# Optimization experiments

Measured on AMD Instinct MI355X. Metric: run time of the kernel, lower is better.

## Reference

```python
import jax, jax.numpy as jnp
import numpy as np

B, S, HID = 2, 2048, 2048
H, D = 16, 128        # num_heads, kv_channels
LAYER_IDX = 4
MASK_VALUE = -10000.0


def setup_inputs() -> dict:
    key = jax.random.key(0)
    ks = jax.random.split(key, 5)
    hidden_states = jax.random.normal(ks[0], (B, S, HID), dtype=jnp.float32)
    # causal mask, broadcastable to [B, q, H, k] per torch.where(mask, w, mask_value)
    causal = jnp.tril(jnp.ones((S, S), dtype=bool))
    attention_mask = jnp.broadcast_to(causal[None, :, None, :], (B, S, 1, S))
    Wq = jax.random.normal(ks[1], (HID, H * D), dtype=jnp.float32) * (HID ** -0.5)
    bq = jnp.zeros((H * D,), dtype=jnp.float32)
    Wkv = jax.random.normal(ks[2], (HID, 2 * D), dtype=jnp.float32) * (HID ** -0.5)
    bkv = jnp.zeros((2 * D,), dtype=jnp.float32)
    Wp = jax.random.normal(ks[3], (H * D, HID), dtype=jnp.float32) * ((H * D) ** -0.5)
    bp = jnp.zeros((HID,), dtype=jnp.float32)
    return {"hidden_states": hidden_states, "attention_mask": attention_mask,
            "Wq": Wq, "bq": bq, "Wkv": Wkv, "bkv": bkv, "Wp": Wp, "bp": bp}


def reference(hidden_states, attention_mask, Wq, bq, Wkv, bkv, Wp, bp):
    # projections
    q = hidden_states @ Wq + bq                      # [B,S,H*D]
    kv = hidden_states @ Wkv + bkv                   # [B,S,2D]
    k, v = kv[..., :D], kv[..., D:]                  # shared single K/V head [B,S,D]
    qh = q.reshape(B, S, H, D)
    # baddbmm with alpha = 1/(layer_idx * sqrt(D))
    scale_factor = (1.0 / LAYER_IDX) / (D ** 0.5)
    scores = jnp.einsum('bqhd,bkd->bqhk', qh, k) * scale_factor  # [B,q,H,k]
    # upcast softmax with unscale = layer_idx, masked with -1e4
    scores = scores.astype(jnp.float32) * LAYER_IDX
    scores = jnp.where(attention_mask, scores, MASK_VALUE)
    weights = jax.nn.softmax(scores, axis=-1).astype(hidden_states.dtype)
    attn = jnp.einsum('bqhk,bkd->bqhd', weights, v).reshape(B, S, H * D)
    out = attn @ Wp + bp
    return out
```

## Files before the change

kernel.cpp:

```cpp
#include <hip/hip_runtime.h>

#define DEVI __device__ __forceinline__

typedef unsigned int u32;
typedef unsigned short u16;

constexpr int Bc = 2, Sc = 2048, HIDc = 2048, Hc = 16, Dc = 128;
constexpr int Mrows = Bc * Sc;
constexpr float SCALE = 0.08838834764831845f;
constexpr float M0 = 16.0f;

typedef float f32x4 __attribute__((ext_vector_type(4)));
typedef __bf16 bf16x8 __attribute__((ext_vector_type(8)));

DEVI float bf2f(u16 v) { return __builtin_bit_cast(float, (u32)v << 16); }
DEVI u16 f2bf(float x) {
  u32 u = __builtin_bit_cast(u32, x);
  u32 r = (u + 0x7fffu + ((u >> 16) & 1u)) >> 16;
  return (u16)r;
}

DEVI void async16(void* lds, const void* g) {
  __builtin_amdgcn_global_load_lds((const __attribute__((address_space(1))) void*)g,
                                   (__attribute__((address_space(3))) void*)lds,
                                   16, 0, 0);
}

constexpr int PRE_BLOCKS = 6289;
constexpr int TS = 66;

DEVI void do_transpose64(const void* in, u16* out, int R, int C, int c0, int r0, bool bf,
                         u16* tile, int tid) {
  const int cg = (tid & 7) * 8, ry = tid >> 3;
#pragma unroll
  for (int p = 0; p < 2; ++p) {
    int r = ry + p * 32;
    size_t idx = (size_t)(r0 + r) * C + (c0 + cg);
    u16 tmp[8];
    if (bf) {
      *(uint4*)tmp = *(const uint4*)&((const u16*)in)[idx];
    } else {
      const float* f = (const float*)in + idx;
#pragma unroll
      for (int j = 0; j < 8; ++j) tmp[j] = f2bf(f[j]);
    }
    *(uint4*)&tile[r * TS + cg] = *(const uint4*)tmp;
  }
  __syncthreads();
  const int rx = (tid & 7) * 8, cy = tid >> 3;
#pragma unroll
  for (int p = 0; p < 2; ++p) {
    int c = cy + p * 32;
    u16 tmp[8];
#pragma unroll
    for (int j = 0; j < 8; ++j) tmp[j] = tile[(rx + j) * TS + c];
    *(uint4*)&out[(size_t)(c0 + c) * R + r0 + rx] = *(const uint4*)tmp;
  }
}

__global__ __launch_bounds__(256) void pre_kernel(const void* __restrict__ hs,
                                                  const void* __restrict__ Wq,
                                                  const void* __restrict__ bq,
                                                  const void* __restrict__ Wkv,
                                                  const void* __restrict__ bkv,
                                                  const void* __restrict__ Wp,
                                                  const void* __restrict__ bp,
                                                  u16* __restrict__ HSb, u16* __restrict__ WqT,
                                                  u16* __restrict__ WkvT, u16* __restrict__ WpT,
                                                  u16* __restrict__ biasB, int* __restrict__ flag) {
  __shared__ int cnt;
  __shared__ u16 tile[64 * TS];
  const int tid = threadIdx.x, bx = blockIdx.x;
  if (tid == 0) cnt = 0;
  __syncthreads();
  int ok = 0;
  const u32* hw = (const u32*)hs;
  for (int i = tid; i < 512; i += 256) {
    u32 lo = hw[i] & 0xffffu;
    u32 e = (lo >> 7) & 0xffu;
    if (lo == 0u || (e >= 118u && e <= 134u)) ok++;
  }
  atomicAdd(&cnt, ok);
  __syncthreads();
  const bool bf = cnt > 256;
  if (bx == 0 && tid == 0) *flag = bf ? 1 : 0;

  if (bx < 4096) {
    int i = (bx * 256 + tid) * 8;
    if (bf) {
      *(uint4*)&HSb[i] = *(const uint4*)&((const u16*)hs)[i];
    } else {
      const float* f = (const float*)hs;
      u16 tmp[8];
#pragma unroll
      for (int j = 0; j < 8; ++j) tmp[j] = f2bf(f[i + j]);
      *(uint4*)&HSb[i] = *(const uint4*)tmp;
    }
  } else if (bx < 5120) {
    int t = bx - 4096;
    do_transpose64(Wq, WqT, 2048, 2048, (t & 31) * 64, (t >> 5) * 64, bf, tile, tid);
  } else if (bx < 5248) {
    int t = bx - 5120;
    do_transpose64(Wkv, WkvT, 2048, 256, (t & 3) * 64, (t >> 2) * 64, bf, tile, tid);
  } else if (bx < 6272) {
    int t = bx - 5248;
    do_transpose64(Wp, WpT, 2048, 2048, (t & 31) * 64, (t >> 5) * 64, bf, tile, tid);
  } else {
    int i = (bx - 6272) * 256 + tid;
    if (i < 4352) {
      const void* src;
      int j;
      if (i < 2048) { src = bq; j = i; }
      else if (i < 2304) { src = bkv; j = i - 2048; }
      else { src = bp; j = i - 2304; }
      biasB[i] = bf ? ((const u16*)src)[j] : f2bf(((const float*)src)[j]);
    }
  }
}

__global__ __launch_bounds__(512, 4) void gemm_bt(const u16* __restrict__ A,
                                                  const u16* __restrict__ BT,
                                                  const u16* __restrict__ bias,
                                                  void* __restrict__ C,
                                                  int M, int N, int K,
                                                  const int* __restrict__ flag,
                                                  int mode) {
  __shared__ __align__(16) u16 As[2][128 * 32];
  __shared__ __align__(16) u16 Bs[2][128 * 32];
  const int tid = threadIdx.x;
  const int bm = blockIdx.x, bn = blockIdx.y;
  const int wave = tid >> 6, lane = tid & 63;
  const int wm = (wave & 3) * 32, wn = (wave >> 2) * 64;
  const int lr = lane & 15, kq = lane >> 4;
  f32x4 acc[2][4] = {};
  const size_t a_base = (size_t)bm * 128 * K;
  const size_t b_base = (size_t)bn * 128 * K;

#define STAGE(k0, buf)                                                             \
  {                                                                                \
    int r = tid >> 2, c = tid & 3;                                                 \
    int gc = (c ^ (r & 3)) << 3;                                                   \
    async16(&As[buf][tid * 8], A + a_base + (size_t)r * K + (k0) + gc);            \
    async16(&Bs[buf][tid * 8], BT + b_base + (size_t)r * K + (k0) + gc);           \
  }

  STAGE(0, 0);
  const int nsteps = K >> 5;
  for (int s = 0; s < nsteps; ++s) {
    const int cur = s & 1;
    asm volatile("s_waitcnt vmcnt(0)" ::: "memory");
    asm volatile("s_barrier" ::: "memory");
    if (s + 1 < nsteps) STAGE((s + 1) << 5, cur ^ 1);
    bf16x8 af[2], bfr[4];
#pragma unroll
    for (int i = 0; i < 2; ++i) {
      int ra = wm + i * 16 + lr;
      af[i] = *(const bf16x8*)&As[cur][ra * 32 + ((kq ^ (ra & 3)) << 3)];
    }
#pragma unroll
    for (int i = 0; i < 4; ++i) {
      int rb = wn + i * 16 + lr;
      bfr[i] = *(const bf16x8*)&Bs[cur][rb * 32 + ((kq ^ (rb & 3)) << 3)];
    }
#pragma unroll
    for (int mi = 0; mi < 2; ++mi)
#pragma unroll
      for (int ni = 0; ni < 4; ++ni)
        acc[mi][ni] = __builtin_amdgcn_mfma_f32_16x16x32_bf16(af[mi], bfr[ni], acc[mi][ni], 0, 0, 0);
  }
#undef STAGE

  if (mode == 3) {
    u16* Qout = (u16*)C;
    u16* KsG = Qout + (size_t)4096 * 2048;
    u16* VtG = KsG + (size_t)4096 * 128;
    const bool isQ = (bn < 16);
#pragma unroll
    for (int mi = 0; mi < 2; ++mi)
#pragma unroll
      for (int ni = 0; ni < 4; ++ni) {
        int col = bn * 128 + wn + ni * 16 + lr;
        float bv = bf2f(bias[col]);
#pragma unroll
        for (int rr = 0; rr < 4; ++rr) {
          int row = bm * 128 + wm + mi * 16 + kq * 4 + rr;
          u16 v = f2bf(acc[mi][ni][rr] + bv);
          if (isQ) {
            Qout[(size_t)row * 2048 + col] = v;
          } else {
            int c2 = col - 2048;
            if (c2 < 128) {
              int d = c2;
              KsG[(size_t)row * 128 + (((d >> 3) ^ (row & 15)) << 3) + (d & 7)] = v;
            } else {
              int d = c2 - 128, bb = row >> 11, s = row & 2047;
              VtG[((size_t)(bb * 128 + d)) * 2048 + (s & ~63) +
                  ((((s >> 3) & 7) ^ (d & 7)) << 3) + (s & 7)] = v;
            }
          }
        }
      }
    return;
  }
  const bool out16 = (mode == 0) || (*flag != 0);
#pragma unroll
  for (int mi = 0; mi < 2; ++mi)
#pragma unroll
    for (int ni = 0; ni < 4; ++ni) {
      int col = bn * 128 + wn + ni * 16 + lr;
      float bv = bf2f(bias[col]);
#pragma unroll
      for (int rr = 0; rr < 4; ++rr) {
        int row = bm * 128 + wm + mi * 16 + kq * 4 + rr;
        float v = acc[mi][ni][rr] + bv;
        size_t idx = (size_t)row * N + col;
        if (out16) ((u16*)C)[idx] = f2bf(v);
        else ((float*)C)[idx] = v;
      }
    }
}

constexpr int PS_STRIDE = 72;

__global__ __launch_bounds__(256) void flash_mfma(const u16* __restrict__ Q,
                                                  const u16* __restrict__ KsG,
                                                  const u16* __restrict__ VtG,
                                                  u16* __restrict__ O) {
  __shared__ __align__(16) u16 Ks[2][64 * 128];
  __shared__ __align__(16) u16 Vt[2][128 * 64];
  __shared__ __align__(16) u16 Ps[64 * PS_STRIDE];
  const int pairidx = blockIdx.x, h = blockIdx.y, b = blockIdx.z;
  const int tid = threadIdx.x;
  const int wave = tid >> 6, lane = tid & 63;
  const int lr = lane & 15, kq = lane >> 4;

  for (int half = 0; half < 2; ++half) {
    const int qt = (half == 0) ? pairidx : 31 - pairidx;
    bf16x8 qf[4];
    const u16* qbase = Q + ((size_t)(b * 2048 + qt * 64 + wave * 16 + lr)) * 2048 + h * 128;
#pragma unroll
    for (int kk = 0; kk < 4; ++kk)
      qf[kk] = *(const bf16x8*)(qbase + kk * 32 + kq * 8);
    f32x4 of[8] = {};
    float lsum[4] = {0.f, 0.f, 0.f, 0.f};
    const int srow = qt * 64 + wave * 16 + kq * 4;
    const int kmax = qt * 64;

    {
      const u16* g = KsG + ((size_t)(b * 2048)) * 128;
#pragma unroll
      for (int it = 0; it < 4; ++it)
        async16(&Ks[0][it * 2048 + tid * 8], g + it * 2048 + tid * 8);
      const size_t vbase = ((size_t)b * 128) * 2048;
#pragma unroll
      for (int it = 0; it < 4; ++it) {
        int chunk = it * 256 + tid;
        async16(&Vt[0][chunk * 8], VtG + vbase + (size_t)(chunk >> 3) * 2048 + (chunk & 7) * 8);
      }
    }

    for (int k0 = 0; k0 <= kmax; k0 += 64) {
      const int cur = (k0 >> 6) & 1;
      asm volatile("s_waitcnt vmcnt(0)" ::: "memory");
      asm volatile("s_barrier" ::: "memory");
      if (k0 + 64 <= kmax) {
        const int nxt = cur ^ 1;
        const u16* g = KsG + ((size_t)(b * 2048 + k0 + 64)) * 128;
#pragma unroll
        for (int it = 0; it < 4; ++it)
          async16(&Ks[nxt][it * 2048 + tid * 8], g + it * 2048 + tid * 8);
        const size_t vbase = ((size_t)b * 128) * 2048 + k0 + 64;
#pragma unroll
        for (int it = 0; it < 4; ++it) {
          int chunk = it * 256 + tid;
          async16(&Vt[nxt][chunk * 8], VtG + vbase + (size_t)(chunk >> 3) * 2048 + (chunk & 7) * 8);
        }
      }

      const bool diag = (k0 == kmax);
      f32x4 sf[4] = {};
#pragma unroll
      for (int nt = 0; nt < 4; ++nt) {
        int keyl = nt * 16 + lr;
#pragma unroll
        for (int kk = 0; kk < 4; ++kk) {
          const bf16x8 kf = *(const bf16x8*)&Ks[cur][keyl * 128 + ((((kk << 2) + kq) ^ lr) << 3)];
          sf[nt] = __builtin_amdgcn_mfma_f32_16x16x32_bf16(qf[kk], kf, sf[nt], 0, 0, 0);
        }
      }
#pragma unroll
      for (int nt = 0; nt < 4; ++nt) {
        int t = k0 + nt * 16 + lr;
#pragma unroll
        for (int r = 0; r < 4; ++r) {
          float v = fmaf(sf[nt][r], SCALE, -M0);
          if (diag && t > srow + r) v = -1e30f;
          float p = __expf(v);
          lsum[r] += p;
          Ps[(wave * 16 + kq * 4 + r) * PS_STRIDE + nt * 16 + lr] = f2bf(p);
        }
      }
#pragma unroll
      for (int ks = 0; ks < 2; ++ks) {
        const bf16x8 pf = *(const bf16x8*)&Ps[(wave * 16 + lr) * PS_STRIDE + ks * 32 + kq * 8];
#pragma unroll
        for (int dt = 0; dt < 8; ++dt) {
          int d = dt * 16 + lr;
          const bf16x8 vf = *(const bf16x8*)&Vt[cur][d * 64 + ((((ks << 2) + kq) ^ (d & 7)) << 3)];
          of[dt] = __builtin_amdgcn_mfma_f32_16x16x32_bf16(pf, vf, of[dt], 0, 0, 0);
        }
      }
    }
    float linv[4];
#pragma unroll
    for (int r = 0; r < 4; ++r) {
      float l = lsum[r];
      l += __shfl_xor(l, 1);
      l += __shfl_xor(l, 2);
      l += __shfl_xor(l, 4);
      l += __shfl_xor(l, 8);
      linv[r] = 1.f / l;
    }
    u16* obase = O + ((size_t)(b * 2048 + qt * 64 + wave * 16 + kq * 4)) * 2048 + h * 128;
#pragma unroll
    for (int dt = 0; dt < 8; ++dt)
#pragma unroll
      for (int r = 0; r < 4; ++r)
        obase[(size_t)r * 2048 + dt * 16 + lr] = f2bf(of[dt][r] * linv[r]);
    __syncthreads();
  }
}

extern "C" void kernel_launch(void* const* d_in, const int* in_sizes, int n_in,
                              void* d_out, int out_size, void* d_ws, size_t ws_size,
                              hipStream_t stream) {
  (void)in_sizes; (void)n_in; (void)out_size; (void)ws_size;
  const void* hs  = d_in[0];
  const void* Wq  = d_in[2];
  const void* bq  = d_in[3];
  const void* Wkv = d_in[4];
  const void* bkv = d_in[5];
  const void* Wp  = d_in[6];
  const void* bp  = d_in[7];

  char* ws = (char*)d_ws;
  int* flag  = (int*)(ws + 0);
  u16* HSb   = (u16*)(ws + 256);
  u16* WqT   = (u16*)(ws + 16777472);
  u16* WkvT  = (u16*)(ws + 25166080);
  u16* WpT   = (u16*)(ws + 26214656);
  u16* biasB = (u16*)(ws + 34603264);
  u16* Qb    = (u16*)(ws + 34611968);
  u16* KsG   = (u16*)(ws + 51389184);
  u16* VtG   = (u16*)(ws + 52437760);
  u16* ATTNb = (u16*)(ws + 53486336);

  pre_kernel<<<PRE_BLOCKS, 256, 0, stream>>>(hs, Wq, bq, Wkv, bkv, Wp, bp,
                                             HSb, WqT, WkvT, WpT, biasB, flag);
  gemm_bt<<<dim3(32, 18), 512, 0, stream>>>(HSb, WqT, biasB, Qb, 4096, 2304, 2048, flag, 3);
  flash_mfma<<<dim3(16, 16, 2), 256, 0, stream>>>(Qb, KsG, VtG, ATTNb);
  gemm_bt<<<dim3(32, 16), 512, 0, stream>>>(ATTNb, WpT, biasB + 2304, d_out, 4096, 2048, 2048, flag, 1);
}
```

Before: 311.3 us.

## Enlarge flash attention query tile to 128 rows per block

Each wave now processes two 16-row query slices (32 rows), so a block covers 128 query rows and every K/V tile loaded into LDS feeds twice as many MFMAs. The grid is halved to 8x16x2 blocks with causal pairing adjusted, and the diagonal masking now spans the last two key tiles. This cuts K/V LDS traffic and global reloads per query row, at the cost of doubled accumulator registers (launch_bounds min 1) and fewer blocks for occupancy and load balance.

New measurement: 328.2 us. 1.05x slower.

```diff
diff --git a/kernel.cpp b/kernel.cpp
--- a/kernel.cpp
+++ b/kernel.cpp
@@ -222,29 +222,35 @@
 
 constexpr int PS_STRIDE = 72;
 
-__global__ __launch_bounds__(256) void flash_mfma(const u16* __restrict__ Q,
-                                                  const u16* __restrict__ KsG,
-                                                  const u16* __restrict__ VtG,
-                                                  u16* __restrict__ O) {
+__global__ __launch_bounds__(256, 1) void flash_mfma(const u16* __restrict__ Q,
+                                                     const u16* __restrict__ KsG,
+                                                     const u16* __restrict__ VtG,
+                                                     u16* __restrict__ O) {
   __shared__ __align__(16) u16 Ks[2][64 * 128];
   __shared__ __align__(16) u16 Vt[2][128 * 64];
-  __shared__ __align__(16) u16 Ps[64 * PS_STRIDE];
+  __shared__ __align__(16) u16 Ps[128 * PS_STRIDE];
   const int pairidx = blockIdx.x, h = blockIdx.y, b = blockIdx.z;
   const int tid = threadIdx.x;
   const int wave = tid >> 6, lane = tid & 63;
   const int lr = lane & 15, kq = lane >> 4;
+  const int wm = wave * 32;
 
   for (int half = 0; half < 2; ++half) {
-    const int qt = (half == 0) ? pairidx : 31 - pairidx;
-    bf16x8 qf[4];
-    const u16* qbase = Q + ((size_t)(b * 2048 + qt * 64 + wave * 16 + lr)) * 2048 + h * 128;
-#pragma unroll
-    for (int kk = 0; kk < 4; ++kk)
-      qf[kk] = *(const bf16x8*)(qbase + kk * 32 + kq * 8);
-    f32x4 of[8] = {};
-    float lsum[4] = {0.f, 0.f, 0.f, 0.f};
-    const int srow = qt * 64 + wave * 16 + kq * 4;
-    const int kmax = qt * 64;
+    const int qt = (half == 0) ? pairidx : 15 - pairidx;
+    bf16x8 qf[2][4];
+#pragma unroll
+    for (int mi = 0; mi < 2; ++mi) {
+      const u16* qbase =
+          Q + ((size_t)(b * 2048 + qt * 128 + wm + mi * 16 + lr)) * 2048 + h * 128;
+#pragma unroll
+      for (int kk = 0; kk < 4; ++kk)
+        qf[mi][kk] = *(const bf16x8*)(qbase + kk * 32 + kq * 8);
+    }
+    f32x4 of[2][8] = {};
+    float lsum[2][4] = {{0.f, 0.f, 0.f, 0.f}, {0.f, 0.f, 0.f, 0.f}};
+    const int srow = qt * 128 + wm + kq * 4;
+    const int kmax = qt * 128 + 64;
+    const int diag0 = qt * 128;
 
     {
       const u16* g = KsG + ((size_t)(b * 2048)) * 128;
@@ -273,60 +279,70 @@
 #pragma unroll
         for (int it = 0; it < 4; ++it) {
           int chunk = it * 256 + tid;
-          async16(&Vt[nxt][chunk * 8], VtG + vbase + (size_t)(chunk >> 3) * 2048 + (chunk & 7) * 8);
-        }
-      }
-
-      const bool diag = (k0 == kmax);
-      f32x4 sf[4] = {};
+          async16(&Vt[nxt][chunk * 8],
+                  VtG + vbase + (size_t)(chunk >> 3) * 2048 + (chunk & 7) * 8);
+        }
+      }
+
+      const bool diag = (k0 >= diag0);
+      f32x4 sf[2][4] = {};
 #pragma unroll
       for (int nt = 0; nt < 4; ++nt) {
         int keyl = nt * 16 + lr;
 #pragma unroll
         for (int kk = 0; kk < 4; ++kk) {
           const bf16x8 kf = *(const bf16x8*)&Ks[cur][keyl * 128 + ((((kk << 2) + kq) ^ lr) << 3)];
-          sf[nt] = __builtin_amdgcn_mfma_f32_16x16x32_bf16(qf[kk], kf, sf[nt], 0, 0, 0);
-        }
-      }
-#pragma unroll
-      for (int nt = 0; nt < 4; ++nt) {
-        int t = k0 + nt * 16 + lr;
-#pragma unroll
-        for (int r = 0; r < 4; ++r) {
-          float v = fmaf(sf[nt][r], SCALE, -M0);
-          if (diag && t > srow + r) v = -1e30f;
-          float p = __expf(v);
-          lsum[r] += p;
-          Ps[(wave * 16 + kq * 4 + r) * PS_STRIDE + nt * 16 + lr] = f2bf(p);
-        }
-      }
+          sf[0][nt] = __builtin_amdgcn_mfma_f32_16x16x32_bf16(qf[0][kk], kf, sf[0][nt], 0, 0, 0);
+          sf[1][nt] = __builtin_amdgcn_mfma_f32_16x16x32_bf16(qf[1][kk], kf, sf[1][nt], 0, 0, 0);
+        }
+      }
+#pragma unroll
+      for (int mi = 0; mi < 2; ++mi)
+#pragma unroll
+        for (int nt = 0; nt < 4; ++nt) {
+          int t = k0 + nt * 16 + lr;
+#pragma unroll
+          for (int r = 0; r < 4; ++r) {
+            float v = fmaf(sf[mi][nt][r], SCALE, -M0);
+            if (diag && t > srow + mi * 16 + r) v = -1e30f;
+            float p = __expf(v);
+            lsum[mi][r] += p;
+            Ps[(wm + mi * 16 + kq * 4 + r) * PS_STRIDE + nt * 16 + lr] = f2bf(p);
+          }
+        }
 #pragma unroll
       for (int ks = 0; ks < 2; ++ks) {
-        const bf16x8 pf = *(const bf16x8*)&Ps[(wave * 16 + lr) * PS_STRIDE + ks * 32 + kq * 8];
+        const bf16x8 pf0 = *(const bf16x8*)&Ps[(wm + lr) * PS_STRIDE + ks * 32 + kq * 8];
+        const bf16x8 pf1 = *(const bf16x8*)&Ps[(wm + 16 + lr) * PS_STRIDE + ks * 32 + kq * 8];
 #pragma unroll
         for (int dt = 0; dt < 8; ++dt) {
           int d = dt * 16 + lr;
           const bf16x8 vf = *(const bf16x8*)&Vt[cur][d * 64 + ((((ks << 2) + kq) ^ (d & 7)) << 3)];
-          of[dt] = __builtin_amdgcn_mfma_f32_16x16x32_bf16(pf, vf, of[dt], 0, 0, 0);
-        }
-      }
-    }
-    float linv[4];
-#pragma unroll
-    for (int r = 0; r < 4; ++r) {
-      float l = lsum[r];
-      l += __shfl_xor(l, 1);
-      l += __shfl_xor(l, 2);
-      l += __shfl_xor(l, 4);
-      l += __shfl_xor(l, 8);
-      linv[r] = 1.f / l;
-    }
-    u16* obase = O + ((size_t)(b * 2048 + qt * 64 + wave * 16 + kq * 4)) * 2048 + h * 128;
-#pragma unroll
-    for (int dt = 0; dt < 8; ++dt)
-#pragma unroll
-      for (int r = 0; r < 4; ++r)
-        obase[(size_t)r * 2048 + dt * 16 + lr] = f2bf(of[dt][r] * linv[r]);
+          of[0][dt] = __builtin_amdgcn_mfma_f32_16x16x32_bf16(pf0, vf, of[0][dt], 0, 0, 0);
+          of[1][dt] = __builtin_amdgcn_mfma_f32_16x16x32_bf16(pf1, vf, of[1][dt], 0, 0, 0);
+        }
+      }
+    }
+#pragma unroll
+    for (int mi = 0; mi < 2; ++mi) {
+      float linv[4];
+#pragma unroll
+      for (int r = 0; r < 4; ++r) {
+        float l = lsum[mi][r];
+        l += __shfl_xor(l, 1);
+        l += __shfl_xor(l, 2);
+        l += __shfl_xor(l, 4);
+        l += __shfl_xor(l, 8);
+        linv[r] = 1.f / l;
+      }
+      u16* obase =
+          O + ((size_t)(b * 2048 + qt * 128 + wm + mi * 16 + kq * 4)) * 2048 + h * 128;
+#pragma unroll
+      for (int dt = 0; dt < 8; ++dt)
+#pragma unroll
+        for (int r = 0; r < 4; ++r)
+          obase[(size_t)r * 2048 + dt * 16 + lr] = f2bf(of[mi][dt][r] * linv[r]);
+    }
     __syncthreads();
   }
 }
@@ -358,6 +374,6 @@
   pre_kernel<<<PRE_BLOCKS, 256, 0, stream>>>(hs, Wq, bq, Wkv, bkv, Wp, bp,
                                              HSb, WqT, WkvT, WpT, biasB, flag);
   gemm_bt<<<dim3(32, 18), 512, 0, stream>>>(HSb, WqT, biasB, Qb, 4096, 2304, 2048, flag, 3);
-  flash_mfma<<<dim3(16, 16, 2), 256, 0, stream>>>(Qb, KsG, VtG, ATTNb);
+  flash_mfma<<<dim3(8, 16, 2), 256, 0, stream>>>(Qb, KsG, VtG, ATTNb);
   gemm_bt<<<dim3(32, 16), 512, 0, stream>>>(ATTNb, WpT, biasB + 2304, d_out, 4096, 2048, 2048, flag, 1);
 }
```

## Keep softmax probabilities in registers via transposed QK MFMA and permuted V layout

Applied to the files above, without the earlier changes.

Swaps the MFMA operand order for QK^T so each lane holds scores for one query row across keys, which lets the probabilities be packed into bf16 registers and fed directly as the A operand of the PV MFMA. This removes the LDS round-trip through the Ps buffer. To make that work, the key order inside V^T is permuted when it is written by the projection kernel. The row-sum reduction and the causal mask index are rewritten to match, and launch bounds now request two blocks per CU.

Result: faster. 297.8 us (-4.3%).

```diff
diff --git a/kernel.cpp b/kernel.cpp
--- a/kernel.cpp
+++ b/kernel.cpp
@@ -194,8 +194,9 @@
               KsG[(size_t)row * 128 + (((d >> 3) ^ (row & 15)) << 3) + (d & 7)] = v;
             } else {
               int d = c2 - 128, bb = row >> 11, s = row & 2047;
-              VtG[((size_t)(bb * 128 + d)) * 2048 + (s & ~63) +
-                  ((((s >> 3) & 7) ^ (d & 7)) << 3) + (s & 7)] = v;
+              int s2 = (s & ~31) | (((s >> 2) & 3) << 3) | (((s >> 4) & 1) << 2) | (s & 3);
+              VtG[((size_t)(bb * 128 + d)) * 2048 + (s2 & ~63) +
+                  ((((s2 >> 3) & 7) ^ (d & 7)) << 3) + (s2 & 7)] = v;
             }
           }
         }
@@ -220,15 +221,12 @@
     }
 }
 
-constexpr int PS_STRIDE = 72;
-
-__global__ __launch_bounds__(256) void flash_mfma(const u16* __restrict__ Q,
-                                                  const u16* __restrict__ KsG,
-                                                  const u16* __restrict__ VtG,
-                                                  u16* __restrict__ O) {
+__global__ __launch_bounds__(256, 2) void flash_mfma(const u16* __restrict__ Q,
+                                                     const u16* __restrict__ KsG,
+                                                     const u16* __restrict__ VtG,
+                                                     u16* __restrict__ O) {
   __shared__ __align__(16) u16 Ks[2][64 * 128];
   __shared__ __align__(16) u16 Vt[2][128 * 64];
-  __shared__ __align__(16) u16 Ps[64 * PS_STRIDE];
   const int pairidx = blockIdx.x, h = blockIdx.y, b = blockIdx.z;
   const int tid = threadIdx.x;
   const int wave = tid >> 6, lane = tid & 63;
@@ -242,8 +240,8 @@
     for (int kk = 0; kk < 4; ++kk)
       qf[kk] = *(const bf16x8*)(qbase + kk * 32 + kq * 8);
     f32x4 of[8] = {};
-    float lsum[4] = {0.f, 0.f, 0.f, 0.f};
-    const int srow = qt * 64 + wave * 16 + kq * 4;
+    float lsum = 0.f;
+    const int rowabs = qt * 64 + wave * 16 + lr;
     const int kmax = qt * 64;
 
     {
@@ -273,7 +271,8 @@
 #pragma unroll
         for (int it = 0; it < 4; ++it) {
           int chunk = it * 256 + tid;
-          async16(&Vt[nxt][chunk * 8], VtG + vbase + (size_t)(chunk >> 3) * 2048 + (chunk & 7) * 8);
+          async16(&Vt[nxt][chunk * 8],
+                  VtG + vbase + (size_t)(chunk >> 3) * 2048 + (chunk & 7) * 8);
         }
       }
 
@@ -285,42 +284,42 @@
 #pragma unroll
         for (int kk = 0; kk < 4; ++kk) {
           const bf16x8 kf = *(const bf16x8*)&Ks[cur][keyl * 128 + ((((kk << 2) + kq) ^ lr) << 3)];
-          sf[nt] = __builtin_amdgcn_mfma_f32_16x16x32_bf16(qf[kk], kf, sf[nt], 0, 0, 0);
+          sf[nt] = __builtin_amdgcn_mfma_f32_16x16x32_bf16(kf, qf[kk], sf[nt], 0, 0, 0);
         }
       }
+      u32 pk[4][2];
 #pragma unroll
       for (int nt = 0; nt < 4; ++nt) {
-        int t = k0 + nt * 16 + lr;
+        float p[4];
 #pragma unroll
         for (int r = 0; r < 4; ++r) {
           float v = fmaf(sf[nt][r], SCALE, -M0);
-          if (diag && t > srow + r) v = -1e30f;
-          float p = __expf(v);
-          lsum[r] += p;
-          Ps[(wave * 16 + kq * 4 + r) * PS_STRIDE + nt * 16 + lr] = f2bf(p);
+          if (diag && (k0 + nt * 16 + kq * 4 + r) > rowabs) v = -1e30f;
+          p[r] = __expf(v);
+          lsum += p[r];
         }
-      }
-#pragma unroll
-      for (int ks = 0; ks < 2; ++ks) {
-        const bf16x8 pf = *(const bf16x8*)&Ps[(wave * 16 + lr) * PS_STRIDE + ks * 32 + kq * 8];
-#pragma unroll
-        for (int dt = 0; dt < 8; ++dt) {
-          int d = dt * 16 + lr;
-          const bf16x8 vf = *(const bf16x8*)&Vt[cur][d * 64 + ((((ks << 2) + kq) ^ (d & 7)) << 3)];
-          of[dt] = __builtin_amdgcn_mfma_f32_16x16x32_bf16(pf, vf, of[dt], 0, 0, 0);
-        }
-      }
-    }
+        asm("v_cvt_pk_bf16_f32 %0, %1, %2" : "=v"(pk[nt][0]) : "v"(p[0]), "v"(p[1]));
+        asm("v_cvt_pk_bf16_f32 %0, %1, %2" : "=v"(pk[nt][1]) : "v"(p[2]), "v"(p[3]));
+      }
+      const uint4 pw0 = {pk[0][0], pk[0][1], pk[1][0], pk[1][1]};
+      const uint4 pw1 = {pk[2][0], pk[2][1], pk[3][0], pk[3][1]};
+      const bf16x8 pf0 = __builtin_bit_cast(bf16x8, pw0);
+      const bf16x8 pf1 = __builtin_bit_cast(bf16x8, pw1);
+#pragma unroll
+      for (int dt = 0; dt < 8; ++dt) {
+        int d = dt * 16 + lr;
+        const bf16x8 vf0 = *(const bf16x8*)&Vt[cur][d * 64 + ((kq ^ (d & 7)) << 3)];
+        of[dt] = __builtin_amdgcn_mfma_f32_16x16x32_bf16(pf0, vf0, of[dt], 0, 0, 0);
+        const bf16x8 vf1 = *(const bf16x8*)&Vt[cur][d * 64 + (((4 + kq) ^ (d & 7)) << 3)];
+        of[dt] = __builtin_amdgcn_mfma_f32_16x16x32_bf16(pf1, vf1, of[dt], 0, 0, 0);
+      }
+    }
+    lsum += __shfl_xor(lsum, 16);
+    lsum += __shfl_xor(lsum, 32);
     float linv[4];
 #pragma unroll
-    for (int r = 0; r < 4; ++r) {
-      float l = lsum[r];
-      l += __shfl_xor(l, 1);
-      l += __shfl_xor(l, 2);
-      l += __shfl_xor(l, 4);
-      l += __shfl_xor(l, 8);
-      linv[r] = 1.f / l;
-    }
+    for (int r = 0; r < 4; ++r)
+      linv[r] = 1.f / __shfl(lsum, kq * 4 + r);
     u16* obase = O + ((size_t)(b * 2048 + qt * 64 + wave * 16 + kq * 4)) * 2048 + h * 128;
 #pragma unroll
     for (int dt = 0; dt < 8; ++dt)
```
